# Optimization experiments

Measured on AMD Instinct MI355X. Metric: run time of the kernel, lower is better.

## Reference

```python
import jax, jax.numpy as jnp
import numpy as np

N, PSI, D = 65536, 1024, 256


def setup_inputs() -> dict:
    key = jax.random.key(0)
    k1, k2 = jax.random.split(key)
    X = jax.random.normal(k1, (N, D), dtype=jnp.float32)
    samples = jax.random.normal(k2, (PSI, D), dtype=jnp.float32)
    sample_weights = jnp.ones((1, PSI), dtype=jnp.float32)  # initializer='ones'
    return {"X": X, "samples": samples, "sample_weights": sample_weights}


def reference(X, samples, sample_weights):
    # Original loop computes, for each codebook row s_i:
    #   (sum((X - s_i)^2, axis=1))^(1/2)   (p=2)
    # which is exactly the Euclidean distance matrix [N, PSI].
    # per-sample loop (same math, one pass instead of PSI kernel launches).
    x2 = jnp.sum(X * X, axis=1, keepdims=True)           # [N, 1]
    s2 = jnp.sum(samples * samples, axis=1)              # [PSI]
    d2 = x2 - 2.0 * (X @ samples.T) + s2[None, :]        # [N, PSI]
    dist = jnp.sqrt(jnp.maximum(d2, 0.0))
    m_dis = dist * sample_weights                        # broadcast [1, PSI]
    # Faithful to original: softmax over axis=0 (across batch rows), soft=True.
    return jax.nn.softmax(-m_dis, axis=0)
```

## Files before the change

### kernel.cpp

```cpp
#include <hip/hip_runtime.h>
#include <hip/hip_bf16.h>
#include <math.h>

#define N_ROWS 65536
#define PSI    1024
#define DDIM   256

typedef _Float16       half8 __attribute__((ext_vector_type(8)));
typedef _Float16       half4 __attribute__((ext_vector_type(4)));
typedef float          f32x4 __attribute__((ext_vector_type(4)));

#define LOG2E 1.4426950408889634f

#if __has_builtin(__builtin_amdgcn_sqrtf)
#define FSQRT(x) __builtin_amdgcn_sqrtf(x)
#else
#define FSQRT(x) sqrtf(x)
#endif
#if __has_builtin(__builtin_amdgcn_exp2f)
#define FEXP2(x) __builtin_amdgcn_exp2f(x)
#else
#define FEXP2(x) exp2f(x)
#endif
#if __has_builtin(__builtin_amdgcn_rcpf)
#define FRCP(x) __builtin_amdgcn_rcpf(x)
#else
#define FRCP(x) (1.0f / (x))
#endif

__device__ __forceinline__ void gload16(const void* g, void* l) {
    __builtin_amdgcn_global_load_lds(
        (const __attribute__((address_space(1))) unsigned int*)g,
        (__attribute__((address_space(3))) unsigned int*)l, 16, 0, 0);
}

__global__ __launch_bounds__(256) void k_convert_all(
    const float* __restrict__ X, const float* __restrict__ S,
    _Float16* __restrict__ Xh, _Float16* __restrict__ Sh,
    float* __restrict__ x2, float* __restrict__ s2,
    float* __restrict__ gsum)
{
    const int bid = blockIdx.x;
    if (bid == 16640) {
        for (int i = threadIdx.x; i < PSI; i += 256) gsum[i] = 0.0f;
        return;
    }
    const float* in; _Float16* outh; float* nrm; int row;
    const int wib  = threadIdx.x >> 6;
    const int lane = threadIdx.x & 63;
    if (bid < 16384) { in = X; outh = Xh; nrm = x2; row = bid * 4 + wib; }
    else { in = S; outh = Sh; nrm = s2; row = (bid - 16384) * 4 + wib; }
    const f32x4 v = __builtin_nontemporal_load(
        (const f32x4*)&in[(size_t)row * DDIM + lane * 4]);
    float s = v[0] * v[0] + v[1] * v[1] + v[2] * v[2] + v[3] * v[3];
    #pragma unroll
    for (int o = 32; o > 0; o >>= 1) s += __shfl_down(s, o);
    if (lane == 0) nrm[row] = s;
    half4 h;
    h[0] = (_Float16)v[0]; h[1] = (_Float16)v[1];
    h[2] = (_Float16)v[2]; h[3] = (_Float16)v[3];
    *(half4*)&outh[(size_t)row * DDIM + lane * 4] = h;
}

template<int MODE>
__global__ __launch_bounds__(512, 2) void k_gemm(
    const _Float16* __restrict__ Xh, const _Float16* __restrict__ Sh,
    const float* __restrict__ x2, const float* __restrict__ s2,
    const float* __restrict__ w,
    float* __restrict__ gsum, float* __restrict__ out)
{
    __shared__ _Float16 As[2][2][128 * 64];
    __shared__ _Float16 Bs[2][2][128 * 64];

    const int tid = threadIdx.x;
    const int wv  = tid >> 6;
    const int wr  = wv >> 2;
    const int wc  = wv & 3;
    const int l15 = tid & 15;
    const int l4  = (tid & 63) >> 4;

    const int fid  = blockIdx.x;
    const int wgid = (fid & 7) * 128 + (fid >> 3);
    const int rowb = wgid >> 2;
    const int row0 = rowb * 256;
    const int col0 = (wgid & 3) * 256;

    f32x4 acc[8][4];
    #pragma unroll
    for (int i = 0; i < 8; ++i)
        #pragma unroll
        for (int j = 0; j < 4; ++j) acc[i][j] = (f32x4){0.f, 0.f, 0.f, 0.f};

    const int grow = tid >> 3;
    const int gch  = (tid & 7) ^ (grow & 7);
    const _Float16* gA = Xh + (size_t)(row0 + grow) * DDIM + gch * 8;
    const _Float16* gB = Sh + (size_t)(col0 + grow) * DDIM + gch * 8;

    auto stageA = [&](int kt, int buf, int h) {
        #pragma unroll
        for (int rg = 0; rg < 2; ++rg)
            gload16(gA + (size_t)(h * 128 + rg * 64) * DDIM + kt * 64,
                    &As[buf][h][(rg * 64 + wv * 8) * 64]);
    };
    auto stageB = [&](int kt, int buf, int h) {
        #pragma unroll
        for (int rg = 0; rg < 2; ++rg)
            gload16(gB + (size_t)(h * 128 + rg * 64) * DDIM + kt * 64,
                    &Bs[buf][h][(rg * 64 + wv * 8) * 64]);
    };

    const int qa0 = l15 * 64 + ((l4)     ^ (l15 & 7)) * 8;
    const int qa1 = l15 * 64 + ((4 + l4) ^ (l15 & 7)) * 8;
    const int bof = (wc & 1) * 4096;

    half8 a[4][2], blo[2][2], bhi[2][2];
    auto loadA = [&](int cur, int hsel) {
        #pragma unroll
        for (int i = 0; i < 4; ++i) {
            a[i][0] = *(const half8*)&As[cur][wr][(hsel * 4 + i) * 1024 + qa0];
            a[i][1] = *(const half8*)&As[cur][wr][(hsel * 4 + i) * 1024 + qa1];
        }
    };
    auto loadB = [&](int cur, half8 b[2][2], int fnb) {
        #pragma unroll
        for (int jn = 0; jn < 2; ++jn) {
            b[jn][0] = *(const half8*)&Bs[cur][wc >> 1][bof + (fnb + jn) * 1024 + qa0];
            b[jn][1] = *(const half8*)&Bs[cur][wc >> 1][bof + (fnb + jn) * 1024 + qa1];
        }
    };
    auto mfmaQ = [&](half8 b[2][2], int fmb, int fnb) {
        __builtin_amdgcn_s_setprio(1);
        #pragma unroll
        for (int i = 0; i < 4; ++i)
            #pragma unroll
            for (int jn = 0; jn < 2; ++jn)
                #pragma unroll
                for (int kk = 0; kk < 2; ++kk)
                    acc[fmb + i][fnb + jn] = __builtin_amdgcn_mfma_f32_16x16x32_f16(
                        a[i][kk], b[jn][kk], acc[fmb + i][fnb + jn], 0, 0, 0);
        __builtin_amdgcn_s_setprio(0);
    };

    stageA(0, 0, 0); stageA(0, 0, 1); stageB(0, 0, 0); stageB(0, 0, 1);
    asm volatile("s_waitcnt vmcnt(0)\ns_barrier" ::: "memory");

    #pragma unroll
    for (int t = 0; t < 4; ++t) {
        const int cur = t & 1, nxt = cur ^ 1;
        loadA(cur, 0); loadB(cur, blo, 0);
        if (t < 3) stageA(t + 1, nxt, 0);
        asm volatile("s_barrier" ::: "memory");
        mfmaQ(blo, 0, 0);
        asm volatile("s_barrier" ::: "memory");
        loadB(cur, bhi, 2);
        if (t < 3) stageA(t + 1, nxt, 1);
        asm volatile("s_barrier" ::: "memory");
        mfmaQ(bhi, 0, 2);
        asm volatile("s_barrier" ::: "memory");
        loadA(cur, 1);
        if (t < 3) stageB(t + 1, nxt, 0);
        asm volatile("s_barrier" ::: "memory");
        mfmaQ(bhi, 4, 2);
        asm volatile("s_barrier" ::: "memory");
        if (t < 3) stageB(t + 1, nxt, 1);
        asm volatile("s_barrier" ::: "memory");
        mfmaQ(blo, 4, 0);
        if (t < 3) asm volatile("s_waitcnt vmcnt(0)\ns_barrier" ::: "memory");
    }
    __syncthreads();

    float4 x2r[8];
    #pragma unroll
    for (int fm = 0; fm < 8; ++fm)
        x2r[fm] = *(const float4*)&x2[row0 + wr * 128 + fm * 16 + l4 * 4];

    if (MODE == 0) {
        float* s_sm = (float*)&As[0][0][0];
        if (tid < 256) s_sm[tid] = 0.0f;
        __syncthreads();
        #pragma unroll
        for (int fn = 0; fn < 4; ++fn) {
            const int cl = wc * 64 + fn * 16 + l15;
            const int c  = col0 + cl;
            const float s2c = s2[c], ww2 = w[c] * LOG2E;
            float s = 0.0f;
            #pragma unroll
            for (int fm = 0; fm < 8; ++fm) {
                const float* xr = (const float*)&x2r[fm];
                #pragma unroll
                for (int j = 0; j < 4; ++j) {
                    float d2 = xr[j] + s2c - 2.0f * acc[fm][fn][j];
                    s += FEXP2(-FSQRT(fmaxf(d2, 0.0f)) * ww2);
                }
            }
            s += __shfl_xor(s, 16);
            s += __shfl_xor(s, 32);
            if (l4 == 0) atomicAdd(&s_sm[cl], s);
        }
        __syncthreads();
        if (tid < 256) atomicAdd(&gsum[col0 + tid], s_sm[tid]);
    } else {
        #pragma unroll
        for (int fn = 0; fn < 4; ++fn) {
            const int c = col0 + wc * 64 + fn * 16 + l15;
            const float s2c = s2[c], ww2 = w[c] * LOG2E;
            const float rsc = FRCP(gsum[c]);
            #pragma unroll
            for (int fm = 0; fm < 8; ++fm) {
                const float* xr = (const float*)&x2r[fm];
                const int rbase = row0 + wr * 128 + fm * 16 + l4 * 4;
                #pragma unroll
                for (int j = 0; j < 4; ++j) {
                    float d2 = xr[j] + s2c - 2.0f * acc[fm][fn][j];
                    float u  = FEXP2(-FSQRT(fmaxf(d2, 0.0f)) * ww2) * rsc;
                    __builtin_nontemporal_store(u, &out[(size_t)(rbase + j) * PSI + c]);
                }
            }
        }
    }
}

extern "C" void kernel_launch(void* const* d_in, const int* in_sizes, int n_in,
                              void* d_out, int out_size, void* d_ws, size_t ws_size,
                              hipStream_t stream) {
    const float* X = (const float*)d_in[0];
    const float* S = (const float*)d_in[1];
    const float* w = (const float*)d_in[2];
    float* out = (float*)d_out;

    char* ws = (char*)d_ws;
    _Float16* Xh   = (_Float16*)(ws);
    _Float16* Sh   = (_Float16*)(ws + 33554432);
    float*    x2   = (float*)   (ws + 34078720);
    float*    s2   = (float*)   (ws + 34340864);
    float*    gsum = (float*)   (ws + 34344960);

    k_convert_all<<<dim3(16641), dim3(256), 0, stream>>>(
        X, S, Xh, Sh, x2, s2, gsum);
    k_gemm<0><<<dim3(1024), dim3(512), 0, stream>>>(
        Xh, Sh, x2, s2, w, gsum, nullptr);
    k_gemm<1><<<dim3(1024), dim3(512), 0, stream>>>(
        Xh, Sh, x2, s2, w, gsum, out);
}
```

Baseline: 154.5 us.

## Make GEMM blocks persistent over all column tiles and grid-stride conversion

Each GEMM workgroup now owns one 256-row stripe and loops over all four column tiles, prefetching the next tile's A and B during the last k-step so the pipeline keeps running across tiles. The grid shrinks from 1024 to 256 blocks, which cuts launch and prologue cost, lets x2 be loaded once per block, and allows A reuse through cache. The conversion kernel becomes grid-stride with 2048 blocks. The trade-off is 256 blocks of 512 threads, which may not fill all CUs well and lengthens the serial work per block.

```diff
diff --git a/kernel.cpp b/kernel.cpp
--- a/kernel.cpp
+++ b/kernel.cpp
@@ -40,26 +40,26 @@
     float* __restrict__ x2, float* __restrict__ s2,
     float* __restrict__ gsum)
 {
-    const int bid = blockIdx.x;
-    if (bid == 16640) {
-        for (int i = threadIdx.x; i < PSI; i += 256) gsum[i] = 0.0f;
-        return;
-    }
-    const float* in; _Float16* outh; float* nrm; int row;
     const int wib  = threadIdx.x >> 6;
     const int lane = threadIdx.x & 63;
-    if (bid < 16384) { in = X; outh = Xh; nrm = x2; row = bid * 4 + wib; }
-    else { in = S; outh = Sh; nrm = s2; row = (bid - 16384) * 4 + wib; }
-    const f32x4 v = __builtin_nontemporal_load(
-        (const f32x4*)&in[(size_t)row * DDIM + lane * 4]);
-    float s = v[0] * v[0] + v[1] * v[1] + v[2] * v[2] + v[3] * v[3];
-    #pragma unroll
-    for (int o = 32; o > 0; o >>= 1) s += __shfl_down(s, o);
-    if (lane == 0) nrm[row] = s;
-    half4 h;
-    h[0] = (_Float16)v[0]; h[1] = (_Float16)v[1];
-    h[2] = (_Float16)v[2]; h[3] = (_Float16)v[3];
-    *(half4*)&outh[(size_t)row * DDIM + lane * 4] = h;
+    for (int u = blockIdx.x; u < 16640; u += 2048) {
+        const float* in; _Float16* outh; float* nrm; int row;
+        if (u < 16384) { in = X; outh = Xh; nrm = x2; row = u * 4 + wib; }
+        else { in = S; outh = Sh; nrm = s2; row = (u - 16384) * 4 + wib; }
+        const f32x4 v = __builtin_nontemporal_load(
+            (const f32x4*)&in[(size_t)row * DDIM + lane * 4]);
+        float s = v[0] * v[0] + v[1] * v[1] + v[2] * v[2] + v[3] * v[3];
+        #pragma unroll
+        for (int o = 32; o > 0; o >>= 1) s += __shfl_down(s, o);
+        if (lane == 0) nrm[row] = s;
+        half4 h;
+        h[0] = (_Float16)v[0]; h[1] = (_Float16)v[1];
+        h[2] = (_Float16)v[2]; h[3] = (_Float16)v[3];
+        *(half4*)&outh[(size_t)row * DDIM + lane * 4] = h;
+    }
+    if (blockIdx.x == 0) {
+        for (int i = threadIdx.x; i < PSI; i += 256) gsum[i] = 0.0f;
+    }
 }
 
 template<int MODE>
@@ -71,6 +71,7 @@
 {
     __shared__ _Float16 As[2][2][128 * 64];
     __shared__ _Float16 Bs[2][2][128 * 64];
+    __shared__ float    s_sm[256];
 
     const int tid = threadIdx.x;
     const int wv  = tid >> 6;
@@ -79,11 +80,8 @@
     const int l15 = tid & 15;
     const int l4  = (tid & 63) >> 4;
 
-    const int fid  = blockIdx.x;
-    const int wgid = (fid & 7) * 128 + (fid >> 3);
-    const int rowb = wgid >> 2;
+    const int rowb = (blockIdx.x & 7) * 32 + (blockIdx.x >> 3);
     const int row0 = rowb * 256;
-    const int col0 = (wgid & 3) * 256;
 
     f32x4 acc[8][4];
     #pragma unroll
@@ -94,7 +92,7 @@
     const int grow = tid >> 3;
     const int gch  = (tid & 7) ^ (grow & 7);
     const _Float16* gA = Xh + (size_t)(row0 + grow) * DDIM + gch * 8;
-    const _Float16* gB = Sh + (size_t)(col0 + grow) * DDIM + gch * 8;
+    const _Float16* gB = Sh + (size_t)grow * DDIM + gch * 8;
 
     auto stageA = [&](int kt, int buf, int h) {
         #pragma unroll
@@ -102,10 +100,10 @@
             gload16(gA + (size_t)(h * 128 + rg * 64) * DDIM + kt * 64,
                     &As[buf][h][(rg * 64 + wv * 8) * 64]);
     };
-    auto stageB = [&](int kt, int buf, int h) {
+    auto stageB = [&](int ct, int kt, int buf, int h) {
         #pragma unroll
         for (int rg = 0; rg < 2; ++rg)
-            gload16(gB + (size_t)(h * 128 + rg * 64) * DDIM + kt * 64,
+            gload16(gB + (size_t)(ct * 256 + h * 128 + rg * 64) * DDIM + kt * 64,
                     &Bs[buf][h][(rg * 64 + wv * 8) * 64]);
     };
 
@@ -141,81 +139,99 @@
         __builtin_amdgcn_s_setprio(0);
     };
 
-    stageA(0, 0, 0); stageA(0, 0, 1); stageB(0, 0, 0); stageB(0, 0, 1);
-    asm volatile("s_waitcnt vmcnt(0)\ns_barrier" ::: "memory");
-
-    #pragma unroll
-    for (int t = 0; t < 4; ++t) {
-        const int cur = t & 1, nxt = cur ^ 1;
-        loadA(cur, 0); loadB(cur, blo, 0);
-        if (t < 3) stageA(t + 1, nxt, 0);
-        asm volatile("s_barrier" ::: "memory");
-        mfmaQ(blo, 0, 0);
-        asm volatile("s_barrier" ::: "memory");
-        loadB(cur, bhi, 2);
-        if (t < 3) stageA(t + 1, nxt, 1);
-        asm volatile("s_barrier" ::: "memory");
-        mfmaQ(bhi, 0, 2);
-        asm volatile("s_barrier" ::: "memory");
-        loadA(cur, 1);
-        if (t < 3) stageB(t + 1, nxt, 0);
-        asm volatile("s_barrier" ::: "memory");
-        mfmaQ(bhi, 4, 2);
-        asm volatile("s_barrier" ::: "memory");
-        if (t < 3) stageB(t + 1, nxt, 1);
-        asm volatile("s_barrier" ::: "memory");
-        mfmaQ(blo, 4, 0);
-        if (t < 3) asm volatile("s_waitcnt vmcnt(0)\ns_barrier" ::: "memory");
-    }
-    __syncthreads();
-
     float4 x2r[8];
     #pragma unroll
     for (int fm = 0; fm < 8; ++fm)
         x2r[fm] = *(const float4*)&x2[row0 + wr * 128 + fm * 16 + l4 * 4];
 
-    if (MODE == 0) {
-        float* s_sm = (float*)&As[0][0][0];
-        if (tid < 256) s_sm[tid] = 0.0f;
-        __syncthreads();
-        #pragma unroll
-        for (int fn = 0; fn < 4; ++fn) {
-            const int cl = wc * 64 + fn * 16 + l15;
-            const int c  = col0 + cl;
-            const float s2c = s2[c], ww2 = w[c] * LOG2E;
-            float s = 0.0f;
-            #pragma unroll
-            for (int fm = 0; fm < 8; ++fm) {
-                const float* xr = (const float*)&x2r[fm];
-                #pragma unroll
-                for (int j = 0; j < 4; ++j) {
-                    float d2 = xr[j] + s2c - 2.0f * acc[fm][fn][j];
-                    s += FEXP2(-FSQRT(fmaxf(d2, 0.0f)) * ww2);
+    stageA(0, 0, 0); stageA(0, 0, 1); stageB(0, 0, 0, 0); stageB(0, 0, 0, 1);
+
+    #pragma unroll 1
+    for (int ct = 0; ct < 4; ++ct) {
+        if (MODE == 0 || ct == 0)
+            asm volatile("s_waitcnt vmcnt(0)\ns_barrier" ::: "memory");
+        else
+            asm volatile("s_waitcnt vmcnt(32)\ns_barrier" ::: "memory");
+
+        #pragma unroll
+        for (int t = 0; t < 4; ++t) {
+            const int cur = t & 1, nxt = cur ^ 1;
+            loadA(cur, 0); loadB(cur, blo, 0);
+            if (t < 3) stageA(t + 1, nxt, 0);
+            else if (ct < 3) stageA(0, nxt, 0);
+            asm volatile("s_barrier" ::: "memory");
+            mfmaQ(blo, 0, 0);
+            asm volatile("s_barrier" ::: "memory");
+            loadB(cur, bhi, 2);
+            if (t < 3) stageA(t + 1, nxt, 1);
+            else if (ct < 3) stageA(0, nxt, 1);
+            asm volatile("s_barrier" ::: "memory");
+            mfmaQ(bhi, 0, 2);
+            asm volatile("s_barrier" ::: "memory");
+            loadA(cur, 1);
+            if (t < 3) stageB(ct, t + 1, nxt, 0);
+            else if (ct < 3) stageB(ct + 1, 0, nxt, 0);
+            asm volatile("s_barrier" ::: "memory");
+            mfmaQ(bhi, 4, 2);
+            asm volatile("s_barrier" ::: "memory");
+            if (t < 3) stageB(ct, t + 1, nxt, 1);
+            else if (ct < 3) stageB(ct + 1, 0, nxt, 1);
+            asm volatile("s_barrier" ::: "memory");
+            mfmaQ(blo, 4, 0);
+            if (t < 3) asm volatile("s_waitcnt vmcnt(0)\ns_barrier" ::: "memory");
+        }
+
+        const int col0 = ct * 256;
+        if (MODE == 0) {
+            if (tid < 256) s_sm[tid] = 0.0f;
+            asm volatile("s_waitcnt lgkmcnt(0)\ns_barrier" ::: "memory");
+            #pragma unroll
+            for (int fn = 0; fn < 4; ++fn) {
+                const int cl = wc * 64 + fn * 16 + l15;
+                const int c  = col0 + cl;
+                const float s2c = s2[c], ww2 = w[c] * LOG2E;
+                float s = 0.0f;
+                #pragma unroll
+                for (int fm = 0; fm < 8; ++fm) {
+                    const float* xr = (const float*)&x2r[fm];
+                    #pragma unroll
+                    for (int j = 0; j < 4; ++j) {
+                        float d2 = xr[j] + s2c - 2.0f * acc[fm][fn][j];
+                        s += FEXP2(-FSQRT(fmaxf(d2, 0.0f)) * ww2);
+                    }
+                }
+                s += __shfl_xor(s, 16);
+                s += __shfl_xor(s, 32);
+                if (l4 == 0) atomicAdd(&s_sm[cl], s);
+            }
+            asm volatile("s_waitcnt lgkmcnt(0)\ns_barrier" ::: "memory");
+            if (tid < 256) atomicAdd(&gsum[col0 + tid], s_sm[tid]);
+        } else {
+            #pragma unroll
+            for (int fn = 0; fn < 4; ++fn) {
+                const int c = col0 + wc * 64 + fn * 16 + l15;
+                const float s2c = s2[c], ww2 = w[c] * LOG2E;
+                const float rsc = FRCP(gsum[c]);
+                #pragma unroll
+                for (int fm = 0; fm < 8; ++fm) {
+                    const float* xr = (const float*)&x2r[fm];
+                    const int rbase = row0 + wr * 128 + fm * 16 + l4 * 4;
+                    #pragma unroll
+                    for (int j = 0; j < 4; ++j) {
+                        float d2 = xr[j] + s2c - 2.0f * acc[fm][fn][j];
+                        float u  = FEXP2(-FSQRT(fmaxf(d2, 0.0f)) * ww2) * rsc;
+                        __builtin_nontemporal_store(u,
+                            &out[(size_t)(rbase + j) * PSI + c]);
+                    }
                 }
             }
-            s += __shfl_xor(s, 16);
-            s += __shfl_xor(s, 32);
-            if (l4 == 0) atomicAdd(&s_sm[cl], s);
-        }
-        __syncthreads();
-        if (tid < 256) atomicAdd(&gsum[col0 + tid], s_sm[tid]);
-    } else {
-        #pragma unroll
-        for (int fn = 0; fn < 4; ++fn) {
-            const int c = col0 + wc * 64 + fn * 16 + l15;
-            const float s2c = s2[c], ww2 = w[c] * LOG2E;
-            const float rsc = FRCP(gsum[c]);
-            #pragma unroll
-            for (int fm = 0; fm < 8; ++fm) {
-                const float* xr = (const float*)&x2r[fm];
-                const int rbase = row0 + wr * 128 + fm * 16 + l4 * 4;
-                #pragma unroll
-                for (int j = 0; j < 4; ++j) {
-                    float d2 = xr[j] + s2c - 2.0f * acc[fm][fn][j];
-                    float u  = FEXP2(-FSQRT(fmaxf(d2, 0.0f)) * ww2) * rsc;
-                    __builtin_nontemporal_store(u, &out[(size_t)(rbase + j) * PSI + c]);
-                }
-            }
+        }
+
+        if (ct < 3) {
+            #pragma unroll
+            for (int i = 0; i < 8; ++i)
+                #pragma unroll
+                for (int j = 0; j < 4; ++j) acc[i][j] = (f32x4){0.f, 0.f, 0.f, 0.f};
         }
     }
 }
@@ -235,10 +251,10 @@
     float*    s2   = (float*)   (ws + 34340864);
     float*    gsum = (float*)   (ws + 34344960);
 
-    k_convert_all<<<dim3(16641), dim3(256), 0, stream>>>(
+    k_convert_all<<<dim3(2048), dim3(256), 0, stream>>>(
         X, S, Xh, Sh, x2, s2, gsum);
-    k_gemm<0><<<dim3(1024), dim3(512), 0, stream>>>(
+    k_gemm<0><<<dim3(256), dim3(512), 0, stream>>>(
         Xh, Sh, x2, s2, w, gsum, nullptr);
-    k_gemm<1><<<dim3(1024), dim3(512), 0, stream>>>(
+    k_gemm<1><<<dim3(256), dim3(512), 0, stream>>>(
         Xh, Sh, x2, s2, w, gsum, out);
 }
```

Result: slower. 250.3 us (+62.0%).

## Use smaller-tile output GEMM kernel and grid-stride convert kernel

Applied to the files above, without the earlier changes.

The second (output-writing) pass is split into its own kernel with 128x128 tiles, 256 threads and a simple double-buffered K loop, launched on 4096 blocks instead of 1024 large 256x256 blocks. The aim is better occupancy and store/compute overlap for the write-heavy pass. The sum pass keeps the large-tile kernel. The convert kernel now uses a persistent grid-stride loop over 2048 blocks instead of one block per 4 rows, which cuts block launch overhead. Smaller tiles mean more redundant operand loads from L2.

```diff
diff --git a/kernel.cpp b/kernel.cpp
--- a/kernel.cpp
+++ b/kernel.cpp
@@ -40,34 +40,32 @@
     float* __restrict__ x2, float* __restrict__ s2,
     float* __restrict__ gsum)
 {
-    const int bid = blockIdx.x;
-    if (bid == 16640) {
-        for (int i = threadIdx.x; i < PSI; i += 256) gsum[i] = 0.0f;
-        return;
-    }
-    const float* in; _Float16* outh; float* nrm; int row;
     const int wib  = threadIdx.x >> 6;
     const int lane = threadIdx.x & 63;
-    if (bid < 16384) { in = X; outh = Xh; nrm = x2; row = bid * 4 + wib; }
-    else { in = S; outh = Sh; nrm = s2; row = (bid - 16384) * 4 + wib; }
-    const f32x4 v = __builtin_nontemporal_load(
-        (const f32x4*)&in[(size_t)row * DDIM + lane * 4]);
-    float s = v[0] * v[0] + v[1] * v[1] + v[2] * v[2] + v[3] * v[3];
-    #pragma unroll
-    for (int o = 32; o > 0; o >>= 1) s += __shfl_down(s, o);
-    if (lane == 0) nrm[row] = s;
-    half4 h;
-    h[0] = (_Float16)v[0]; h[1] = (_Float16)v[1];
-    h[2] = (_Float16)v[2]; h[3] = (_Float16)v[3];
-    *(half4*)&outh[(size_t)row * DDIM + lane * 4] = h;
-}
-
-template<int MODE>
-__global__ __launch_bounds__(512, 2) void k_gemm(
+    for (int u = blockIdx.x; u < 16640; u += 2048) {
+        const float* in; _Float16* outh; float* nrm; int row;
+        if (u < 16384) { in = X; outh = Xh; nrm = x2; row = u * 4 + wib; }
+        else { in = S; outh = Sh; nrm = s2; row = (u - 16384) * 4 + wib; }
+        const f32x4 v = __builtin_nontemporal_load(
+            (const f32x4*)&in[(size_t)row * DDIM + lane * 4]);
+        float s = v[0] * v[0] + v[1] * v[1] + v[2] * v[2] + v[3] * v[3];
+        #pragma unroll
+        for (int o = 32; o > 0; o >>= 1) s += __shfl_down(s, o);
+        if (lane == 0) nrm[row] = s;
+        half4 h;
+        h[0] = (_Float16)v[0]; h[1] = (_Float16)v[1];
+        h[2] = (_Float16)v[2]; h[3] = (_Float16)v[3];
+        *(half4*)&outh[(size_t)row * DDIM + lane * 4] = h;
+    }
+    if (blockIdx.x == 0) {
+        for (int i = threadIdx.x; i < PSI; i += 256) gsum[i] = 0.0f;
+    }
+}
+
+__global__ __launch_bounds__(512, 2) void k_gemm_sum(
     const _Float16* __restrict__ Xh, const _Float16* __restrict__ Sh,
     const float* __restrict__ x2, const float* __restrict__ s2,
-    const float* __restrict__ w,
-    float* __restrict__ gsum, float* __restrict__ out)
+    const float* __restrict__ w, float* __restrict__ gsum)
 {
     __shared__ _Float16 As[2][2][128 * 64];
     __shared__ _Float16 Bs[2][2][128 * 64];
@@ -174,47 +172,125 @@
     for (int fm = 0; fm < 8; ++fm)
         x2r[fm] = *(const float4*)&x2[row0 + wr * 128 + fm * 16 + l4 * 4];
 
-    if (MODE == 0) {
-        float* s_sm = (float*)&As[0][0][0];
-        if (tid < 256) s_sm[tid] = 0.0f;
-        __syncthreads();
-        #pragma unroll
-        for (int fn = 0; fn < 4; ++fn) {
-            const int cl = wc * 64 + fn * 16 + l15;
-            const int c  = col0 + cl;
-            const float s2c = s2[c], ww2 = w[c] * LOG2E;
-            float s = 0.0f;
-            #pragma unroll
-            for (int fm = 0; fm < 8; ++fm) {
-                const float* xr = (const float*)&x2r[fm];
+    float* s_sm = (float*)&As[0][0][0];
+    if (tid < 256) s_sm[tid] = 0.0f;
+    __syncthreads();
+    #pragma unroll
+    for (int fn = 0; fn < 4; ++fn) {
+        const int cl = wc * 64 + fn * 16 + l15;
+        const int c  = col0 + cl;
+        const float s2c = s2[c], ww2 = w[c] * LOG2E;
+        float s = 0.0f;
+        #pragma unroll
+        for (int fm = 0; fm < 8; ++fm) {
+            const float* xr = (const float*)&x2r[fm];
+            #pragma unroll
+            for (int j = 0; j < 4; ++j) {
+                float d2 = xr[j] + s2c - 2.0f * acc[fm][fn][j];
+                s += FEXP2(-FSQRT(fmaxf(d2, 0.0f)) * ww2);
+            }
+        }
+        s += __shfl_xor(s, 16);
+        s += __shfl_xor(s, 32);
+        if (l4 == 0) atomicAdd(&s_sm[cl], s);
+    }
+    __syncthreads();
+    if (tid < 256) atomicAdd(&gsum[col0 + tid], s_sm[tid]);
+}
+
+__global__ __launch_bounds__(256) void k_gemm_out(
+    const _Float16* __restrict__ Xh, const _Float16* __restrict__ Sh,
+    const float* __restrict__ x2, const float* __restrict__ s2,
+    const float* __restrict__ w,
+    const float* __restrict__ gsum, float* __restrict__ out)
+{
+    __shared__ _Float16 As[2][128 * 64];
+    __shared__ _Float16 Bs[2][128 * 64];
+
+    const int tid  = threadIdx.x;
+    const int wv   = tid >> 6;
+    const int wr   = wv >> 1;
+    const int wc   = wv & 1;
+    const int l15  = tid & 15;
+    const int l4   = (tid & 63) >> 4;
+
+    const int fid   = blockIdx.x;
+    const int wgid  = (fid & 7) * 512 + (fid >> 3);
+    const int rowb  = wgid >> 3;
+    const int row0  = rowb * 128;
+    const int col0  = (wgid & 7) * 128;
+
+    f32x4 acc[4][4];
+    #pragma unroll
+    for (int i = 0; i < 4; ++i)
+        #pragma unroll
+        for (int j = 0; j < 4; ++j) acc[i][j] = (f32x4){0.f, 0.f, 0.f, 0.f};
+
+    const int srow = tid >> 3;
+    const int skq  = ((tid & 7) ^ (srow & 7)) * 8;
+    const _Float16* gAp = Xh + (size_t)(row0 + srow) * DDIM + skq;
+    const _Float16* gBp = Sh + (size_t)(col0 + srow) * DDIM + skq;
+
+    auto stage = [&](int k0, int b) {
+        _Float16* Ab = &As[b][wv * 512];
+        _Float16* Bb = &Bs[b][wv * 512];
+        #pragma unroll
+        for (int rg = 0; rg < 4; ++rg)
+            gload16(gAp + (size_t)(rg * 32) * DDIM + k0, Ab + rg * 2048);
+        #pragma unroll
+        for (int rg = 0; rg < 4; ++rg)
+            gload16(gBp + (size_t)(rg * 32) * DDIM + k0, Bb + rg * 2048);
+    };
+
+    auto compute = [&](int b) {
+        #pragma unroll
+        for (int kk = 0; kk < 2; ++kk) {
+            half8 af[4], bf[4];
+            #pragma unroll
+            for (int f = 0; f < 4; ++f) {
+                const int swz = (l15 & 7) << 3;
+                const int ha = ((wr * 64 + f * 16 + l15) * 64 + kk * 32 + l4 * 8) ^ swz;
+                const int hb = ((wc * 64 + f * 16 + l15) * 64 + kk * 32 + l4 * 8) ^ swz;
+                af[f] = *(const half8*)&As[b][ha];
+                bf[f] = *(const half8*)&Bs[b][hb];
+            }
+            #pragma unroll
+            for (int fm = 0; fm < 4; ++fm)
                 #pragma unroll
-                for (int j = 0; j < 4; ++j) {
-                    float d2 = xr[j] + s2c - 2.0f * acc[fm][fn][j];
-                    s += FEXP2(-FSQRT(fmaxf(d2, 0.0f)) * ww2);
-                }
-            }
-            s += __shfl_xor(s, 16);
-            s += __shfl_xor(s, 32);
-            if (l4 == 0) atomicAdd(&s_sm[cl], s);
-        }
-        __syncthreads();
-        if (tid < 256) atomicAdd(&gsum[col0 + tid], s_sm[tid]);
-    } else {
-        #pragma unroll
-        for (int fn = 0; fn < 4; ++fn) {
-            const int c = col0 + wc * 64 + fn * 16 + l15;
-            const float s2c = s2[c], ww2 = w[c] * LOG2E;
-            const float rsc = FRCP(gsum[c]);
-            #pragma unroll
-            for (int fm = 0; fm < 8; ++fm) {
-                const float* xr = (const float*)&x2r[fm];
-                const int rbase = row0 + wr * 128 + fm * 16 + l4 * 4;
-                #pragma unroll
-                for (int j = 0; j < 4; ++j) {
-                    float d2 = xr[j] + s2c - 2.0f * acc[fm][fn][j];
-                    float u  = FEXP2(-FSQRT(fmaxf(d2, 0.0f)) * ww2) * rsc;
-                    __builtin_nontemporal_store(u, &out[(size_t)(rbase + j) * PSI + c]);
-                }
+                for (int fn = 0; fn < 4; ++fn)
+                    acc[fm][fn] = __builtin_amdgcn_mfma_f32_16x16x32_f16(
+                        af[fm], bf[fn], acc[fm][fn], 0, 0, 0);
+        }
+    };
+
+    stage(0, 0);
+    __syncthreads();
+    #pragma unroll
+    for (int t = 0; t < 4; ++t) {
+        if (t < 3) stage((t + 1) * 64, (t + 1) & 1);
+        compute(t & 1);
+        if (t < 3) __syncthreads();
+    }
+
+    float4 x2r[4];
+    #pragma unroll
+    for (int fm = 0; fm < 4; ++fm)
+        x2r[fm] = *(const float4*)&x2[row0 + wr * 64 + fm * 16 + l4 * 4];
+
+    #pragma unroll
+    for (int fn = 0; fn < 4; ++fn) {
+        const int c = col0 + wc * 64 + fn * 16 + l15;
+        const float s2c = s2[c], ww2 = w[c] * LOG2E;
+        const float rsc = FRCP(gsum[c]);
+        #pragma unroll
+        for (int fm = 0; fm < 4; ++fm) {
+            const float* xr = (const float*)&x2r[fm];
+            const int rbase = row0 + wr * 64 + fm * 16 + l4 * 4;
+            #pragma unroll
+            for (int j = 0; j < 4; ++j) {
+                float d2 = xr[j] + s2c - 2.0f * acc[fm][fn][j];
+                float u  = FEXP2(-FSQRT(fmaxf(d2, 0.0f)) * ww2) * rsc;
+                __builtin_nontemporal_store(u, &out[(size_t)(rbase + j) * PSI + c]);
             }
         }
     }
@@ -235,10 +311,10 @@
     float*    s2   = (float*)   (ws + 34340864);
     float*    gsum = (float*)   (ws + 34344960);
 
-    k_convert_all<<<dim3(16641), dim3(256), 0, stream>>>(
+    k_convert_all<<<dim3(2048), dim3(256), 0, stream>>>(
         X, S, Xh, Sh, x2, s2, gsum);
-    k_gemm<0><<<dim3(1024), dim3(512), 0, stream>>>(
-        Xh, Sh, x2, s2, w, gsum, nullptr);
-    k_gemm<1><<<dim3(1024), dim3(512), 0, stream>>>(
+    k_gemm_sum<<<dim3(1024), dim3(512), 0, stream>>>(
+        Xh, Sh, x2, s2, w, gsum);
+    k_gemm_out<<<dim3(4096), dim3(256), 0, stream>>>(
         Xh, Sh, x2, s2, w, gsum, out);
 }
```

Result: faster. 147.7 us (-4.4%).
